# Kernel optimization log

Hardware: AMD Instinct MI355X
Metric: run time of the kernel (lower is better)

Reference implementation:

```python
import jax, jax.numpy as jnp
import numpy as np

DIM = 192
SCALE = DIM ** (-0.5)


def setup_inputs() -> dict:
    key = jax.random.key(0)
    qkv = jax.random.normal(key, (8, 4096, 3 * DIM), dtype=jnp.float32)
    return {"qkv": qkv}


def reference(qkv):
    # qkv: [B, T, 3C] -> q, k, v each [B, T, C]
    q, k, v = jnp.split(qkv, 3, axis=2)
    # scale_in=True: scale q and k before distance computation
    q = q * SCALE
    k = k * SCALE
    # L2-distance attention logits: -||q_t - k_s||_2, computed via the
    # expansion ||q||^2 + ||k||^2 - 2 q.k (same as torch.cdist for large inputs)
    q2 = jnp.sum(q * q, axis=-1)          # [B, T]
    k2 = jnp.sum(k * k, axis=-1)          # [B, S]
    d2 = q2[:, :, None] + k2[:, None, :] - 2.0 * jnp.einsum('btc,bsc->bts', q, k)
    d2 = jnp.maximum(d2, 0.0)
    # safe sqrt (zero distance on the diagonal since q and k come from same tokens)
    dist = jnp.where(d2 > 0, jnp.sqrt(jnp.where(d2 > 0, d2, 1.0)), 0.0)
    attn_logits = -dist                    # [B, T, S]
    attn = jax.nn.softmax(attn_logits, axis=-1)
    return jnp.einsum('bts,bsc->btc', attn, v)  # [B, T, C]
```

## Files before the change

kernel.cpp:

```cpp
#include <hip/hip_runtime.h>
#include <hip/hip_bf16.h>


#define BB 8
#define TT 4096
#define CD 192

typedef __attribute__((ext_vector_type(8))) short short8;
typedef __attribute__((ext_vector_type(4))) float float4v;
typedef __attribute__((ext_vector_type(2))) unsigned int uint2v;

constexpr float A2C = (float)(2.0813689810056077 / 192.0);

static __device__ __forceinline__ unsigned short f2bf(float f) {
  unsigned u = __builtin_bit_cast(unsigned, f);
  unsigned r = u + 0x7fffu + ((u >> 16) & 1u);
  return (unsigned short)(r >> 16);
}
static __device__ __forceinline__ float bf2f(unsigned short b) {
  return __builtin_bit_cast(float, (unsigned)b << 16);
}

__global__ __launch_bounds__(256) void prep(
    const float* __restrict__ qkv, short8* __restrict__ qsw,
    short8* __restrict__ ksw, short8* __restrict__ vsw,
    float* __restrict__ q2, float* __restrict__ k2,
    float* __restrict__ out) {
  {
    float4v* o4 = (float4v*)out;
    int base = blockIdx.x * 256 + threadIdx.x;
#pragma unroll
    for (int j = 0; j < 6; ++j)
      o4[base + j * 262144] = (float4v){0.f, 0.f, 0.f, 0.f};
  }

  __shared__ unsigned short tile[32 * 584];
  const int t = threadIdx.x;
  const int b = blockIdx.x >> 7;
  const int sc = blockIdx.x & 127;
  const float* src = qkv + ((size_t)(b * TT + sc * 32)) * (3 * CD);
#pragma unroll
  for (int j = 0; j < 18; ++j) {
    int f = j * 256 + t;
    int row = f / 144, c4 = (f % 144) * 4;
    float4v x = *(const float4v*)(src + (size_t)row * 576 + c4);
    unsigned r0 = (unsigned)f2bf(x[0]) | ((unsigned)f2bf(x[1]) << 16);
    unsigned r1 = (unsigned)f2bf(x[2]) | ((unsigned)f2bf(x[3]) << 16);
    *(uint2v*)&tile[row * 584 + c4] = (uint2v){r0, r1};
  }
  __syncthreads();

  const int lane = t & 63, w = t >> 6;
  const int L = lane & 15, q = lane >> 4;
  const int which = w >> 1;
  const int s16o = w & 1;
  const int row = s16o * 16 + L;
  short8* dst = which ? ksw : qsw;
  const size_t ubase = ((size_t)(b * 256 + sc * 2 + s16o)) * 6;
  float ss = 0.f;
#pragma unroll
  for (int ch = 0; ch < 6; ++ch) {
    short8 fr = *(const short8*)&tile[row * 584 + which * CD + ch * 32 + q * 8];
#pragma unroll
    for (int j = 0; j < 8; ++j) {
      float f = bf2f((unsigned short)fr[j]);
      ss += f * f;
    }
    dst[(ubase + ch) * 64 + lane] = fr;
  }
  ss += __shfl_xor(ss, 16);
  ss += __shfl_xor(ss, 32);
  if (lane < 16)
    (which ? k2 : q2)[b * TT + sc * 32 + s16o * 16 + lane] = ss * A2C;

#pragma unroll
  for (int i = 0; i < 3; ++i) {
    int nt2 = w * 3 + i;
    short8 fr;
#pragma unroll
    for (int j = 0; j < 8; ++j)
      fr[j] = (short)tile[(q * 8 + j) * 584 + 2 * CD + nt2 * 16 + L];
    vsw[((size_t)(b * 12 + nt2) * 128 + sc) * 64 + lane] = fr;
  }
}

__global__ __launch_bounds__(256, 4) void attnh(
    const short8* __restrict__ qsw, const short8* __restrict__ ksw,
    const short8* __restrict__ vsw, const float* __restrict__ q2,
    const float* __restrict__ k2, float* __restrict__ out,
    float* __restrict__ lpart) {
  __shared__ __align__(16) unsigned char s_lds[24576 + 9216];
  float* ldsP = (float*)(s_lds + 24576);

  const int tid = threadIdx.x;
  const int w = tid >> 6;
  const int lane = tid & 63;
  const int L = lane & 15;
  const int q = lane >> 4;
  const int b = blockIdx.x & 7;
  const int qt = (blockIdx.x >> 3) & 63;
  const int sh = blockIdx.x >> 9;
  const int q0 = qt * 64 + w * 16;
  const size_t bT = (size_t)b * TT;
  const int it0 = sh * 64;

  float* pw = ldsP + w * 576;

  auto stageK = [&](int itile) {
    const char* gk = (const char*)(ksw + ((size_t)(b * 256 + 2 * itile)) * 6 * 64);
#pragma unroll
    for (int j = 0; j < 3; ++j) {
      int u = w * 3 + j;
      const char* ga = gk + (u * 64 + lane) * 16;
      char* la = (char*)s_lds + u * 1024;
      __builtin_amdgcn_global_load_lds(
          (const __attribute__((address_space(1))) void*)ga,
          (__attribute__((address_space(3))) void*)la, 16, 0, 0);
    }
  };
  auto stageV = [&](int itile) {
#pragma unroll
    for (int j = 0; j < 3; ++j) {
      int u = w * 3 + j;
      const char* ga = (const char*)vsw +
                       (((size_t)(b * 12 + u) * 128 + itile) * 64 + lane) * 16;
      char* la = (char*)s_lds + 12288 + u * 1024;
      __builtin_amdgcn_global_load_lds(
          (const __attribute__((address_space(1))) void*)ga,
          (__attribute__((address_space(3))) void*)la, 16, 0, 0);
    }
  };

  short8 qf[6];
#pragma unroll
  for (int ch = 0; ch < 6; ++ch)
    qf[ch] = qsw[((size_t)(b * 256 + (q0 >> 4)) * 6 + ch) * 64 + lane];

  float q2l[4];
#pragma unroll
  for (int r = 0; r < 4; ++r) q2l[r] = q2[bT + q0 + 4 * q + r];

  float4v oacc[12];
#pragma unroll
  for (int nt = 0; nt < 12; ++nt) oacc[nt] = (float4v){0.f, 0.f, 0.f, 0.f};
  float lsum[4] = {0.f, 0.f, 0.f, 0.f};

  stageK(it0);
  stageV(it0);
  __syncthreads();

#pragma unroll 1
  for (int it = 0; it < 64; ++it) {
    const int gt = it0 + it;
    const int s0 = gt * 32;

    float k2l[2];
    k2l[0] = k2[bT + s0 + L];
    k2l[1] = k2[bT + s0 + 16 + L];

    float4v sacc[2];
    sacc[0] = (float4v){0.f, 0.f, 0.f, 0.f};
    sacc[1] = (float4v){0.f, 0.f, 0.f, 0.f};
#pragma unroll
    for (int ch = 0; ch < 6; ++ch) {
      short8 kf0 = *(const short8*)(s_lds + ch * 1024 + lane * 16);
      short8 kf1 = *(const short8*)(s_lds + (6 + ch) * 1024 + lane * 16);
      sacc[0] = __builtin_amdgcn_mfma_f32_16x16x32_bf16(qf[ch], kf0, sacc[0], 0, 0, 0);
      sacc[1] = __builtin_amdgcn_mfma_f32_16x16x32_bf16(qf[ch], kf1, sacc[1], 0, 0, 0);
    }

    __syncthreads();
    if (it + 1 < 64) stageK(gt + 1);

#pragma unroll
    for (int nt = 0; nt < 2; ++nt)
#pragma unroll
      for (int r = 0; r < 4; ++r) {
        float dot = sacc[nt][r];
        float tt = fmaf(-2.f * A2C, dot, q2l[r] + k2l[nt]);
        float y = fmaxf(tt, 0.f);
        float p = __builtin_amdgcn_exp2f(-__builtin_amdgcn_sqrtf(y));
        lsum[r] += p;
        pw[(4 * q + r) * 36 + nt * 16 + L] = p;
      }
    float4v p0 = *(const float4v*)(pw + L * 36 + q * 8);
    float4v p1 = *(const float4v*)(pw + L * 36 + q * 8 + 4);
    short8 paf;
#pragma unroll
    for (int j = 0; j < 4; ++j) {
      paf[j] = (short)f2bf(p0[j]);
      paf[j + 4] = (short)f2bf(p1[j]);
    }

#pragma unroll
    for (int nt = 0; nt < 12; ++nt) {
      short8 vf = *(const short8*)(s_lds + 12288 + nt * 1024 + lane * 16);
      oacc[nt] = __builtin_amdgcn_mfma_f32_16x16x32_bf16(paf, vf, oacc[nt], 0, 0, 0);
    }

    __syncthreads();
    if (it + 1 < 64) stageV(gt + 1);
  }

  float* op = out + (bT + q0) * (size_t)CD;
#pragma unroll
  for (int r = 0; r < 4; ++r) {
    float ls = lsum[r];
#pragma unroll
    for (int m = 1; m < 16; m <<= 1) ls += __shfl_xor(ls, m);
    if (L == 0) lpart[(size_t)sh * (BB * TT) + bT + q0 + 4 * q + r] = ls;
#pragma unroll
    for (int nt = 0; nt < 12; ++nt)
      atomicAdd(&op[(size_t)(4 * q + r) * CD + nt * 16 + L], oacc[nt][r]);
  }
}

__global__ __launch_bounds__(256) void combine(
    float* __restrict__ out, const float* __restrict__ lpart) {
  const int idx = blockIdx.x * 256 + threadIdx.x;
  const int row = idx / 48;
  const float inv = 1.f / (lpart[row] + lpart[BB * TT + row]);
  float4v a = ((const float4v*)out)[idx];
#pragma unroll
  for (int j = 0; j < 4; ++j) a[j] *= inv;
  ((float4v*)out)[idx] = a;
}

extern "C" void kernel_launch(void* const* d_in, const int* in_sizes, int n_in,
                              void* d_out, int out_size, void* d_ws, size_t ws_size,
                              hipStream_t stream) {
  (void)in_sizes; (void)n_in; (void)out_size; (void)ws_size;
  const float* qkv = (const float*)d_in[0];
  float* out = (float*)d_out;

  short8* qsw = (short8*)d_ws;
  short8* ksw = qsw + (size_t)BB * 256 * 6 * 64;
  short8* vsw = ksw + (size_t)BB * 256 * 6 * 64;
  float* q2 = (float*)(vsw + (size_t)BB * 12 * 128 * 64);
  float* k2 = q2 + (size_t)BB * TT;
  float* lpart = k2 + (size_t)BB * TT;

  prep<<<BB * 128, 256, 0, stream>>>(qkv, qsw, ksw, vsw, q2, k2, out);
  attnh<<<BB * 128, 256, 0, stream>>>(qsw, ksw, vsw, q2, k2, out, lpart);
  combine<<<BB * TT * 48 / 256, 256, 0, stream>>>(out, lpart);
}
```

Before: 270.3 us.

## Process two query 16-row tiles per wave to reuse staged K/V fragments

Each wave now handles 32 query rows instead of 16, so every K and V fragment read from LDS feeds two MFMAs. The block covers 128 queries, the grid is halved, and the occupancy hint drops from 4 to 2 blocks per SM to make room for the doubled accumulators. This cuts global-to-LDS staging traffic and LDS reads per unit of compute. The cost is higher register pressure and fewer resident waves and blocks (512 blocks on 256 CUs), which reduces latency hiding.

```diff
diff --git a/kernel.cpp b/kernel.cpp
--- a/kernel.cpp
+++ b/kernel.cpp
@@ -84,12 +84,12 @@
   }
 }
 
-__global__ __launch_bounds__(256, 4) void attnh(
+__global__ __launch_bounds__(256, 2) void attnh(
     const short8* __restrict__ qsw, const short8* __restrict__ ksw,
     const short8* __restrict__ vsw, const float* __restrict__ q2,
     const float* __restrict__ k2, float* __restrict__ out,
     float* __restrict__ lpart) {
-  __shared__ __align__(16) unsigned char s_lds[24576 + 9216];
+  __shared__ __align__(16) unsigned char s_lds[24576 + 18432];
   float* ldsP = (float*)(s_lds + 24576);
 
   const int tid = threadIdx.x;
@@ -98,13 +98,13 @@
   const int L = lane & 15;
   const int q = lane >> 4;
   const int b = blockIdx.x & 7;
-  const int qt = (blockIdx.x >> 3) & 63;
-  const int sh = blockIdx.x >> 9;
-  const int q0 = qt * 64 + w * 16;
+  const int qt = (blockIdx.x >> 3) & 31;
+  const int sh = blockIdx.x >> 8;
+  const int q0 = qt * 128 + w * 32;
   const size_t bT = (size_t)b * TT;
   const int it0 = sh * 64;
 
-  float* pw = ldsP + w * 576;
+  float* pw = ldsP + w * 1152;
 
   auto stageK = [&](int itile) {
     const char* gk = (const char*)(ksw + ((size_t)(b * 256 + 2 * itile)) * 6 * 64);
@@ -131,19 +131,28 @@
     }
   };
 
-  short8 qf[6];
-#pragma unroll
-  for (int ch = 0; ch < 6; ++ch)
-    qf[ch] = qsw[((size_t)(b * 256 + (q0 >> 4)) * 6 + ch) * 64 + lane];
-
-  float q2l[4];
-#pragma unroll
-  for (int r = 0; r < 4; ++r) q2l[r] = q2[bT + q0 + 4 * q + r];
-
-  float4v oacc[12];
-#pragma unroll
-  for (int nt = 0; nt < 12; ++nt) oacc[nt] = (float4v){0.f, 0.f, 0.f, 0.f};
-  float lsum[4] = {0.f, 0.f, 0.f, 0.f};
+  short8 qf[2][6];
+#pragma unroll
+  for (int qa = 0; qa < 2; ++qa)
+#pragma unroll
+    for (int ch = 0; ch < 6; ++ch)
+      qf[qa][ch] =
+          qsw[((size_t)(b * 256 + (q0 >> 4) + qa) * 6 + ch) * 64 + lane];
+
+  float q2l[2][4];
+#pragma unroll
+  for (int qa = 0; qa < 2; ++qa)
+#pragma unroll
+    for (int r = 0; r < 4; ++r)
+      q2l[qa][r] = q2[bT + q0 + qa * 16 + 4 * q + r];
+
+  float4v oacc[2][12];
+#pragma unroll
+  for (int qa = 0; qa < 2; ++qa)
+#pragma unroll
+    for (int nt = 0; nt < 12; ++nt)
+      oacc[qa][nt] = (float4v){0.f, 0.f, 0.f, 0.f};
+  float lsum[2][4] = {{0.f, 0.f, 0.f, 0.f}, {0.f, 0.f, 0.f, 0.f}};
 
   stageK(it0);
   stageV(it0);
@@ -158,60 +167,75 @@
     k2l[0] = k2[bT + s0 + L];
     k2l[1] = k2[bT + s0 + 16 + L];
 
-    float4v sacc[2];
-    sacc[0] = (float4v){0.f, 0.f, 0.f, 0.f};
-    sacc[1] = (float4v){0.f, 0.f, 0.f, 0.f};
+    float4v sacc[2][2];
+#pragma unroll
+    for (int qa = 0; qa < 2; ++qa)
+#pragma unroll
+      for (int nt = 0; nt < 2; ++nt)
+        sacc[qa][nt] = (float4v){0.f, 0.f, 0.f, 0.f};
 #pragma unroll
     for (int ch = 0; ch < 6; ++ch) {
       short8 kf0 = *(const short8*)(s_lds + ch * 1024 + lane * 16);
       short8 kf1 = *(const short8*)(s_lds + (6 + ch) * 1024 + lane * 16);
-      sacc[0] = __builtin_amdgcn_mfma_f32_16x16x32_bf16(qf[ch], kf0, sacc[0], 0, 0, 0);
-      sacc[1] = __builtin_amdgcn_mfma_f32_16x16x32_bf16(qf[ch], kf1, sacc[1], 0, 0, 0);
+      sacc[0][0] = __builtin_amdgcn_mfma_f32_16x16x32_bf16(qf[0][ch], kf0, sacc[0][0], 0, 0, 0);
+      sacc[0][1] = __builtin_amdgcn_mfma_f32_16x16x32_bf16(qf[0][ch], kf1, sacc[0][1], 0, 0, 0);
+      sacc[1][0] = __builtin_amdgcn_mfma_f32_16x16x32_bf16(qf[1][ch], kf0, sacc[1][0], 0, 0, 0);
+      sacc[1][1] = __builtin_amdgcn_mfma_f32_16x16x32_bf16(qf[1][ch], kf1, sacc[1][1], 0, 0, 0);
     }
 
     __syncthreads();
     if (it + 1 < 64) stageK(gt + 1);
 
 #pragma unroll
-    for (int nt = 0; nt < 2; ++nt)
-#pragma unroll
-      for (int r = 0; r < 4; ++r) {
-        float dot = sacc[nt][r];
-        float tt = fmaf(-2.f * A2C, dot, q2l[r] + k2l[nt]);
-        float y = fmaxf(tt, 0.f);
-        float p = __builtin_amdgcn_exp2f(-__builtin_amdgcn_sqrtf(y));
-        lsum[r] += p;
-        pw[(4 * q + r) * 36 + nt * 16 + L] = p;
+    for (int qa = 0; qa < 2; ++qa)
+#pragma unroll
+      for (int nt = 0; nt < 2; ++nt)
+#pragma unroll
+        for (int r = 0; r < 4; ++r) {
+          float dot = sacc[qa][nt][r];
+          float tt = fmaf(-2.f * A2C, dot, q2l[qa][r] + k2l[nt]);
+          float y = fmaxf(tt, 0.f);
+          float p = __builtin_amdgcn_exp2f(-__builtin_amdgcn_sqrtf(y));
+          lsum[qa][r] += p;
+          pw[(qa * 16 + 4 * q + r) * 36 + nt * 16 + L] = p;
+        }
+    short8 paf[2];
+#pragma unroll
+    for (int qa = 0; qa < 2; ++qa) {
+      float4v p0 = *(const float4v*)(pw + (qa * 16 + L) * 36 + q * 8);
+      float4v p1 = *(const float4v*)(pw + (qa * 16 + L) * 36 + q * 8 + 4);
+#pragma unroll
+      for (int j = 0; j < 4; ++j) {
+        paf[qa][j] = (short)f2bf(p0[j]);
+        paf[qa][j + 4] = (short)f2bf(p1[j]);
       }
-    float4v p0 = *(const float4v*)(pw + L * 36 + q * 8);
-    float4v p1 = *(const float4v*)(pw + L * 36 + q * 8 + 4);
-    short8 paf;
-#pragma unroll
-    for (int j = 0; j < 4; ++j) {
-      paf[j] = (short)f2bf(p0[j]);
-      paf[j + 4] = (short)f2bf(p1[j]);
     }
 
 #pragma unroll
     for (int nt = 0; nt < 12; ++nt) {
       short8 vf = *(const short8*)(s_lds + 12288 + nt * 1024 + lane * 16);
-      oacc[nt] = __builtin_amdgcn_mfma_f32_16x16x32_bf16(paf, vf, oacc[nt], 0, 0, 0);
+      oacc[0][nt] = __builtin_amdgcn_mfma_f32_16x16x32_bf16(paf[0], vf, oacc[0][nt], 0, 0, 0);
+      oacc[1][nt] = __builtin_amdgcn_mfma_f32_16x16x32_bf16(paf[1], vf, oacc[1][nt], 0, 0, 0);
     }
 
     __syncthreads();
     if (it + 1 < 64) stageV(gt + 1);
   }
 
-  float* op = out + (bT + q0) * (size_t)CD;
-#pragma unroll
-  for (int r = 0; r < 4; ++r) {
-    float ls = lsum[r];
-#pragma unroll
-    for (int m = 1; m < 16; m <<= 1) ls += __shfl_xor(ls, m);
-    if (L == 0) lpart[(size_t)sh * (BB * TT) + bT + q0 + 4 * q + r] = ls;
-#pragma unroll
-    for (int nt = 0; nt < 12; ++nt)
-      atomicAdd(&op[(size_t)(4 * q + r) * CD + nt * 16 + L], oacc[nt][r]);
+#pragma unroll
+  for (int qa = 0; qa < 2; ++qa) {
+    float* op = out + (bT + q0 + qa * 16) * (size_t)CD;
+#pragma unroll
+    for (int r = 0; r < 4; ++r) {
+      float ls = lsum[qa][r];
+#pragma unroll
+      for (int m = 1; m < 16; m <<= 1) ls += __shfl_xor(ls, m);
+      if (L == 0)
+        lpart[(size_t)sh * (BB * TT) + bT + q0 + qa * 16 + 4 * q + r] = ls;
+#pragma unroll
+      for (int nt = 0; nt < 12; ++nt)
+        atomicAdd(&op[(size_t)(4 * q + r) * CD + nt * 16 + L], oacc[qa][nt][r]);
+    }
   }
 }
 
@@ -241,6 +265,6 @@
   float* lpart = k2 + (size_t)BB * TT;
 
   prep<<<BB * 128, 256, 0, stream>>>(qkv, qsw, ksw, vsw, q2, k2, out);
-  attnh<<<BB * 128, 256, 0, stream>>>(qsw, ksw, vsw, q2, k2, out, lpart);
+  attnh<<<BB * 64, 256, 0, stream>>>(qsw, ksw, vsw, q2, k2, out, lpart);
   combine<<<BB * TT * 48 / 256, 256, 0, stream>>>(out, lpart);
 }
```

New measurement: 273.9 us. Within noise of the previous version (+1.3%).
